# Kernel tuning notes

Measured on AMD Instinct MI355X. Metric: run time of the kernel, lower is better.

## Reference

```python
import jax, jax.numpy as jnp
import numpy as np

N = 50000   # nodes in both graphs
E = 800000  # edges per graph
IN = 128
OUT = 64
NEG_SLOPE = 0.2  # DGL GATConv default


def setup_inputs() -> dict:
    key = jax.random.key(0)
    ks = jax.random.split(key, 12)
    stdv = 1.0 / np.sqrt(OUT)
    return {
        'h': jax.random.normal(ks[0], (N, IN), dtype=jnp.float32),
        'src0': jax.random.randint(ks[1], (E,), 0, N, dtype=jnp.int32),
        'dst0': jax.random.randint(ks[2], (E,), 0, N, dtype=jnp.int32),
        'row2': jax.random.randint(ks[3], (E,), 0, N, dtype=jnp.int32),
        'col2': jax.random.randint(ks[4], (E,), 0, N, dtype=jnp.int32),
        'adj_val': jax.random.uniform(ks[5], (E,), dtype=jnp.float32),
        # GATConv params (1 head)
        'W_gat': jax.random.normal(ks[6], (IN, OUT), dtype=jnp.float32) * 0.1,
        'attn_l': jax.random.normal(ks[7], (OUT,), dtype=jnp.float32) * 0.1,
        'attn_r': jax.random.normal(ks[8], (OUT,), dtype=jnp.float32) * 0.1,
        'bias_gat': jnp.zeros((OUT,), dtype=jnp.float32),
        # GraphConvolution params
        'W_gc': jax.random.uniform(ks[9], (IN, OUT), minval=-stdv, maxval=stdv, dtype=jnp.float32),
        'bias_gc': jax.random.uniform(ks[10], (OUT,), minval=-stdv, maxval=stdv, dtype=jnp.float32),
    }


def reference(h, src0, dst0, row2, col2, adj_val, W_gat, attn_l, attn_r, bias_gat, W_gc, bias_gc):
    n = h.shape[0]
    # ---- branch 0: GATConv(1 head) + elu activation ----
    feat = h @ W_gat                        # [N, OUT]
    el = feat @ attn_l                      # [N]
    er = feat @ attn_r                      # [N]
    e = el[src0] + er[dst0]                 # [E]
    e = jnp.where(e > 0, e, NEG_SLOPE * e)  # leaky_relu
    # edge softmax over incoming edges of each dst (stable)
    m = jax.ops.segment_max(e, dst0, num_segments=n)
    ex = jnp.exp(e - m[dst0])
    s = jax.ops.segment_sum(ex, dst0, num_segments=n)
    alpha = ex / s[dst0]                    # [E]
    agg = jax.ops.segment_sum(alpha[:, None] * feat[src0], dst0, num_segments=n)
    z1 = jax.nn.elu(agg + bias_gat)         # [N, OUT]
    # ---- branch 1: GraphConvolution: elu(adj @ (h @ W) + b) ----
    support = h @ W_gc                      # [N, OUT]
    gc = jax.ops.segment_sum(adj_val[:, None] * support[col2], row2, num_segments=n)
    z2 = jax.nn.elu(gc + bias_gc)           # [N, OUT]
    # ---- semantic attention tail (forward is just split+concat) ----
    return jnp.concatenate((z1, z2), axis=1)  # [N, 2*OUT]
```

## Files before the change

kernel.cpp:

```cpp
#include <hip/hip_runtime.h>
#include <hip/hip_bf16.h>
#include <math.h>

#define IN_F 128
#define OUT_F 64
#define BKT_SH 8
#define BKT_MASK 255
#define CHUNK 4096
#define MAXTB 800
#define IDX_BITS 24
#define IDX_MASK ((1u << IDX_BITS) - 1u)
#define PAD 16

typedef __attribute__((ext_vector_type(8))) short bf16x8;
typedef __attribute__((ext_vector_type(4))) float f32x4;

__device__ inline short f2bf(float x) {
    __hip_bfloat16 b = __float2bfloat16(x);
    return *reinterpret_cast<short*>(&b);
}
__device__ inline float bflo(unsigned u) { return __uint_as_float(u << 16); }
__device__ inline float bfhi(unsigned u) { return __uint_as_float(u & 0xffff0000u); }

__global__ __launch_bounds__(256) void k_fused(const float* __restrict__ h,
                                               const float* __restrict__ Wg,
                                               const float* __restrict__ Wc,
                                               const float* __restrict__ attn_l,
                                               const float* __restrict__ attn_r,
                                               __hip_bfloat16* __restrict__ feat,
                                               __hip_bfloat16* __restrict__ support,
                                               float* __restrict__ el,
                                               float* __restrict__ er, int n, int G1,
                                               const int* __restrict__ dst0,
                                               const int* __restrict__ row2,
                                               int* __restrict__ bcnt,
                                               int* __restrict__ chunkhist,
                                               int NB, int E_) {
    __shared__ short Wl[16][128][8];
    __shared__ int hist[MAXTB];

    if ((int)blockIdx.x >= G1) {
        int TB = 2 * NB;
        int t = threadIdx.x;
        int chunk = (int)blockIdx.x - G1;
        for (int i = t; i < TB; i += 256) hist[i] = 0;
        __syncthreads();
        int e0 = chunk * CHUNK;
        for (int i = t; i < CHUNK; i += 256) {
            int e = e0 + i;
            if (e < E_) {
                atomicAdd(&hist[dst0[e] >> BKT_SH], 1);
                atomicAdd(&hist[NB + (row2[e] >> BKT_SH)], 1);
            }
        }
        __syncthreads();
        int* hrow = chunkhist + (size_t)chunk * TB;
        for (int b = t; b < TB; b += 256) {
            int c = hist[b];
            hrow[b] = c;
            if (c) atomicAdd(&bcnt[b * PAD], c);
        }
        return;
    }

    for (int i = threadIdx.x; i < 128 * 32; i += 256) {
        int k = i >> 5;
        int c4 = (i & 31) << 2;
        float4 v4 = (c4 < 64) ? *(const float4*)(Wg + k * 64 + c4)
                              : *(const float4*)(Wc + k * 64 + (c4 - 64));
        short* dst = &Wl[k >> 3][c4][k & 7];
        dst[0]  = f2bf(v4.x);
        dst[8]  = f2bf(v4.y);
        dst[16] = f2bf(v4.z);
        dst[24] = f2bf(v4.w);
    }
    __syncthreads();

    int lane = threadIdx.x & 63;
    int wv = threadIdx.x >> 6;
    int li = lane & 15, lg = lane >> 4;
    int row0 = blockIdx.x * 64 + wv * 16;

    f32x4 acc[8];
#pragma unroll
    for (int ct = 0; ct < 8; ++ct) acc[ct] = (f32x4){0.f, 0.f, 0.f, 0.f};

    int ar = row0 + li;
    if (ar >= n) ar = n - 1;
    const float* hrow = h + (size_t)ar * IN_F + lg * 8;
#pragma unroll
    for (int q = 0; q < 4; ++q) {
        float4 a0 = *(const float4*)(hrow + q * 32);
        float4 a1 = *(const float4*)(hrow + q * 32 + 4);
        bf16x8 af;
        af[0] = f2bf(a0.x); af[1] = f2bf(a0.y); af[2] = f2bf(a0.z); af[3] = f2bf(a0.w);
        af[4] = f2bf(a1.x); af[5] = f2bf(a1.y); af[6] = f2bf(a1.z); af[7] = f2bf(a1.w);
        int kg = q * 4 + lg;
#pragma unroll
        for (int ct = 0; ct < 8; ++ct) {
            bf16x8 bfr = *(const bf16x8*)&Wl[kg][ct * 16 + li][0];
            acc[ct] = __builtin_amdgcn_mfma_f32_16x16x32_bf16(af, bfr, acc[ct], 0, 0, 0);
        }
    }

    float alv[4], arv[4];
#pragma unroll
    for (int ct = 0; ct < 4; ++ct) {
        alv[ct] = attn_l[ct * 16 + li];
        arv[ct] = attn_r[ct * 16 + li];
    }
#pragma unroll
    for (int r = 0; r < 4; ++r) {
        int row = row0 + lg * 4 + r;
        float pl = 0.f, pr = 0.f;
#pragma unroll
        for (int ct = 0; ct < 4; ++ct) {
            pl += acc[ct][r] * alv[ct];
            pr += acc[ct][r] * arv[ct];
        }
#pragma unroll
        for (int m = 8; m; m >>= 1) {
            pl += __shfl_xor(pl, m);
            pr += __shfl_xor(pr, m);
        }
        if (li == 0 && row < n) { el[row] = pl; er[row] = pr; }
    }

#pragma unroll
    for (int r = 0; r < 4; ++r) {
        int row = row0 + lg * 4 + r;
        if (row >= n) continue;
#pragma unroll
        for (int ct = 0; ct < 4; ++ct)
            feat[(size_t)row * OUT_F + ct * 16 + li] = __float2bfloat16(acc[ct][r]);
#pragma unroll
        for (int ct = 4; ct < 8; ++ct)
            support[(size_t)row * OUT_F + (ct - 4) * 16 + li] = __float2bfloat16(acc[ct][r]);
    }
}

__global__ __launch_bounds__(1024) void k_part(const int* __restrict__ src0,
                                               const int* __restrict__ dst0,
                                               const int* __restrict__ row2,
                                               const int* __restrict__ col2,
                                               const float* __restrict__ adj_val,
                                               const float* __restrict__ el,
                                               const float* __restrict__ er,
                                               const int* __restrict__ bcnt,
                                               const int* __restrict__ chunkhist,
                                               int* __restrict__ gfill,
                                               int* __restrict__ boffs,
                                               int* __restrict__ offs, int tot,
                                               int2* __restrict__ tmp,
                                               int NB, int E_, int grand) {
    __shared__ int bo[MAXTB + 1];
    __shared__ int hist[MAXTB];
    __shared__ int rbase[MAXTB];
    __shared__ int sh[1024];
    int TB = 2 * NB;
    int t = threadIdx.x;

    {
        int v = (t < TB) ? bcnt[t * PAD] : 0;
        sh[t] = v;
        __syncthreads();
        for (int off = 1; off < 1024; off <<= 1) {
            int x = (t >= off) ? sh[t - off] : 0;
            __syncthreads();
            sh[t] += x;
            __syncthreads();
        }
        if (t < TB) bo[t] = sh[t] - v;
        if (t == 0) bo[TB] = grand;
    }
    __syncthreads();

    if (blockIdx.x == 0) {
        for (int b = t; b <= TB; b += 1024) boffs[b] = bo[b];
        if (t == 0) offs[tot] = grand;
    }

    const int* hrow = chunkhist + (size_t)blockIdx.x * TB;
    for (int b = t; b < TB; b += 1024) {
        int c = hrow[b];
        int bb = 0;
        if (c) bb = bo[b] + atomicAdd(&gfill[b * PAD], c);
        rbase[b] = bb;
        hist[b] = 0;
    }
    __syncthreads();
    int e0 = blockIdx.x * CHUNK;
    for (int i = t; i < CHUNK; i += 1024) {
        int e = e0 + i;
        if (e < E_) {
            int s = src0[e];
            int d = dst0[e];
            int b = d >> BKT_SH;
            int p = atomicAdd(&hist[b], 1);
            float w = el[s] + er[d];
            w = w > 0.f ? w : 0.2f * w;
            w = __expf(w);
            tmp[(size_t)rbase[b] + p] =
                make_int2((int)(((unsigned)(d & BKT_MASK) << IDX_BITS) | (unsigned)s),
                          __float_as_int(w));
            int r = row2[e];
            int b2 = NB + (r >> BKT_SH);
            int p2 = atomicAdd(&hist[b2], 1);
            tmp[(size_t)rbase[b2] + p2] =
                make_int2((int)(((unsigned)(r & BKT_MASK) << IDX_BITS) | (unsigned)col2[e]),
                          __float_as_int(adj_val[e]));
        }
    }
}

__global__ __launch_bounds__(256) void k_bbuild(const int2* __restrict__ tmp,
                                                const int* __restrict__ boffs,
                                                int* __restrict__ offs,
                                                unsigned* __restrict__ ew, int NB, int n) {
    __shared__ int hcnt[256], hoff[256], hfill[256], sh[256];
    int b = blockIdx.x;
    int t = threadIdx.x;
    int base = boffs[b];
    int cnt = boffs[b + 1] - base;
    bool isGat = b < NB;
    int nodeBase = (isGat ? b : b - NB) << BKT_SH;
    int offsBase = (isGat ? 0 : n) + nodeBase;

    hcnt[t] = 0;
    hfill[t] = 0;
    __syncthreads();
    for (int i = t; i < cnt; i += 256)
        atomicAdd(&hcnt[((unsigned)tmp[(size_t)base + i].x) >> IDX_BITS], 1);
    __syncthreads();
    sh[t] = hcnt[t];
    __syncthreads();
    for (int off = 1; off < 256; off <<= 1) {
        int x = (t >= off) ? sh[t - off] : 0;
        __syncthreads();
        sh[t] += x;
        __syncthreads();
    }
    hoff[t] = sh[t] - hcnt[t];
    if (nodeBase + t < n) offs[offsBase + t] = base + hoff[t];
    __syncthreads();
    for (int i = t; i < cnt; i += 256) {
        int2 v = tmp[(size_t)base + i];
        unsigned loc = ((unsigned)v.x) >> IDX_BITS;
        int p = atomicAdd(&hfill[loc], 1);
        unsigned idx16 = ((unsigned)v.x & IDX_MASK) & 0xffffu;
        unsigned wbits = (unsigned)(unsigned short)f2bf(__int_as_float(v.y));
        ew[(size_t)base + hoff[loc] + p] = (wbits << 16) | idx16;
    }
}

__global__ __launch_bounds__(256) void k_agg(const unsigned* __restrict__ ew,
                                             const int* __restrict__ offs,
                                             const __hip_bfloat16* __restrict__ feat,
                                             const __hip_bfloat16* __restrict__ support,
                                             const float* __restrict__ bias_gat,
                                             const float* __restrict__ bias_gc,
                                             float* __restrict__ out, int n) {
    int wave = (int)(((long long)blockIdx.x * blockDim.x + threadIdx.x) >> 6);
    int lane = threadIdx.x & 63;
    int nq = (n + 3) >> 2;
    if (wave >= 2 * nq) return;
    int q = lane >> 4;
    int fg = lane & 15;
    int qb = q << 4;

    bool isGat = wave < nq;
    int node = (isGat ? wave : wave - nq) * 4 + q;
    bool nodeValid = node < n;
    int wid = (isGat ? 0 : n) + (nodeValid ? node : 0);
    int start = offs[wid];
    int deg = nodeValid ? offs[wid + 1] - start : 0;

    const uint2* fbase = (const uint2*)(isGat ? feat : support);
    float acc[4] = {0.f, 0.f, 0.f, 0.f};
    float sw = 0.f;

    for (int c0 = 0; c0 < deg; c0 += 16) {
        int cnt = min(16, deg - c0);
        bool valid = fg < cnt;
        unsigned e = valid ? ew[(size_t)start + c0 + fg] : 0u;
        float w = bfhi(e);
        float ts = w;
        ts += __shfl_xor(ts, 1);  ts += __shfl_xor(ts, 2);
        ts += __shfl_xor(ts, 4);  ts += __shfl_xor(ts, 8);
        sw += ts;
#pragma unroll 4
        for (int k = 0; k < cnt; ++k) {
            unsigned ek = (unsigned)__shfl((int)e, qb + k);
            float wk = bfhi(ek);
            int ik = (int)(ek & 0xffffu);
            uint2 pv = fbase[(size_t)ik * 16 + fg];
            acc[0] += wk * bflo(pv.x); acc[1] += wk * bfhi(pv.x);
            acc[2] += wk * bflo(pv.y); acc[3] += wk * bfhi(pv.y);
        }
    }
    if (nodeValid) {
        float inv = isGat ? (deg > 0 ? __builtin_amdgcn_rcpf(sw) : 0.f) : 1.f;
        const float* bias = isGat ? bias_gat : bias_gc;
        int outoff = isGat ? 0 : OUT_F;
        float4 bb = *(const float4*)(bias + fg * 4);
        float z0 = acc[0] * inv + bb.x;
        float z1 = acc[1] * inv + bb.y;
        float z2 = acc[2] * inv + bb.z;
        float z3 = acc[3] * inv + bb.w;
        z0 = z0 > 0.f ? z0 : __expf(z0) - 1.f;
        z1 = z1 > 0.f ? z1 : __expf(z1) - 1.f;
        z2 = z2 > 0.f ? z2 : __expf(z2) - 1.f;
        z3 = z3 > 0.f ? z3 : __expf(z3) - 1.f;
        *(float4*)(out + (size_t)node * 128 + outoff + fg * 4) = make_float4(z0, z1, z2, z3);
    }
}

extern "C" void kernel_launch(void* const* d_in, const int* in_sizes, int n_in,
                              void* d_out, int out_size, void* d_ws, size_t ws_size,
                              hipStream_t stream) {
    const float* h        = (const float*)d_in[0];
    const int*   src0     = (const int*)d_in[1];
    const int*   dst0     = (const int*)d_in[2];
    const int*   row2     = (const int*)d_in[3];
    const int*   col2     = (const int*)d_in[4];
    const float* adj_val  = (const float*)d_in[5];
    const float* Wg       = (const float*)d_in[6];
    const float* attn_l   = (const float*)d_in[7];
    const float* attn_r   = (const float*)d_in[8];
    const float* bias_gat = (const float*)d_in[9];
    const float* Wc       = (const float*)d_in[10];
    const float* bias_gc  = (const float*)d_in[11];

    int n  = in_sizes[0] / IN_F;
    int E_ = in_sizes[1];
    float* out = (float*)d_out;

    int NB = (n + BKT_MASK) >> BKT_SH;
    int TB = 2 * NB;
    if (TB > MAXTB) return;
    if (n > 65536) return;
    if (E_ >= (1 << IDX_BITS)) return;

    int nchunk = (E_ + CHUNK - 1) / CHUNK;

    char* p = (char*)d_ws;
    auto alloc = [&](size_t bytes, size_t align) -> void* {
        size_t a = ((size_t)p + align - 1) & ~(align - 1);
        p = (char*)(a + bytes);
        return (void*)a;
    };
    size_t Rbytes = 2 * (size_t)E_ * sizeof(int2);
    if ((size_t)nchunk * TB * sizeof(int) > Rbytes) return;
    char* R = (char*)alloc(Rbytes, 256);
    int*      chunkhist = (int*)R;
    unsigned* ew        = (unsigned*)R;
    int2*  tmp   = (int2*) alloc(2 * (size_t)E_ * sizeof(int2), 256);
    int*   offs  = (int*)  alloc((2 * (size_t)n + 1) * sizeof(int), 16);
    float* el    = (float*)alloc((size_t)n * sizeof(float), 16);
    float* er    = (float*)alloc((size_t)n * sizeof(float), 16);
    int*   bcnt  = (int*)  alloc(2 * (size_t)TB * PAD * sizeof(int), 64);
    int*   gfill = bcnt + TB * PAD;
    int*   boffs = (int*)  alloc(((size_t)TB + 1) * sizeof(int), 16);
    __hip_bfloat16* feat    = (__hip_bfloat16*)alloc((size_t)n * OUT_F * sizeof(__hip_bfloat16), 256);
    __hip_bfloat16* support = (__hip_bfloat16*)alloc((size_t)n * OUT_F * sizeof(__hip_bfloat16), 256);
    size_t need = (size_t)(p - (char*)d_ws);
    if (ws_size < need) return;

    int G1 = (n + 63) / 64;

    hipMemsetAsync(bcnt, 0, 2 * (size_t)TB * PAD * sizeof(int), stream);
    k_fused<<<G1 + nchunk, 256, 0, stream>>>(h, Wg, Wc, attn_l, attn_r,
                                             feat, support, el, er, n, G1,
                                             dst0, row2, bcnt, chunkhist, NB, E_);
    k_part<<<nchunk, 1024, 0, stream>>>(src0, dst0, row2, col2, adj_val,
                                        el, er, bcnt, chunkhist, gfill,
                                        boffs, offs, 2 * n, tmp, NB, E_, 2 * E_);
    k_bbuild<<<TB, 256, 0, stream>>>(tmp, boffs, offs, ew, NB, n);
    int nq = (n + 3) >> 2;
    long long aggthreads = 2LL * nq * 64;
    k_agg<<<(int)((aggthreads + 255) / 256), 256, 0, stream>>>(
        ew, offs, feat, support, bias_gat, bias_gc, out, n);
}
```

Before: 117.0 us.

## Replace global atomic bucket offsets with per-chunk prefix scan; stage bucket build in LDS

Removes the global bcnt/gfill atomics and the memset. Each partition block now recomputes bucket totals and its own per-chunk prefix by reading the whole chunkhist table, which trades atomic contention for redundant reads of about 196x400 ints per block. The GEMM/histogram kernel moves to 512-thread blocks covering 128 rows each. Bucket build now scatters into an LDS buffer and then writes to global memory contiguously, falling back to direct scatter when a bucket is oversized.

```diff
diff --git a/kernel.cpp b/kernel.cpp
--- a/kernel.cpp
+++ b/kernel.cpp
@@ -10,7 +10,7 @@
 #define MAXTB 800
 #define IDX_BITS 24
 #define IDX_MASK ((1u << IDX_BITS) - 1u)
-#define PAD 16
+#define CAPB 6144
 
 typedef __attribute__((ext_vector_type(8))) short bf16x8;
 typedef __attribute__((ext_vector_type(4))) float f32x4;
@@ -22,7 +22,7 @@
 __device__ inline float bflo(unsigned u) { return __uint_as_float(u << 16); }
 __device__ inline float bfhi(unsigned u) { return __uint_as_float(u & 0xffff0000u); }
 
-__global__ __launch_bounds__(256) void k_fused(const float* __restrict__ h,
+__global__ __launch_bounds__(512) void k_fused(const float* __restrict__ h,
                                                const float* __restrict__ Wg,
                                                const float* __restrict__ Wc,
                                                const float* __restrict__ attn_l,
@@ -33,7 +33,6 @@
                                                float* __restrict__ er, int n, int G1,
                                                const int* __restrict__ dst0,
                                                const int* __restrict__ row2,
-                                               int* __restrict__ bcnt,
                                                int* __restrict__ chunkhist,
                                                int NB, int E_) {
     __shared__ short Wl[16][128][8];
@@ -43,10 +42,10 @@
         int TB = 2 * NB;
         int t = threadIdx.x;
         int chunk = (int)blockIdx.x - G1;
-        for (int i = t; i < TB; i += 256) hist[i] = 0;
+        for (int i = t; i < TB; i += 512) hist[i] = 0;
         __syncthreads();
         int e0 = chunk * CHUNK;
-        for (int i = t; i < CHUNK; i += 256) {
+        for (int i = t; i < CHUNK; i += 512) {
             int e = e0 + i;
             if (e < E_) {
                 atomicAdd(&hist[dst0[e] >> BKT_SH], 1);
@@ -55,15 +54,11 @@
         }
         __syncthreads();
         int* hrow = chunkhist + (size_t)chunk * TB;
-        for (int b = t; b < TB; b += 256) {
-            int c = hist[b];
-            hrow[b] = c;
-            if (c) atomicAdd(&bcnt[b * PAD], c);
-        }
+        for (int b = t; b < TB; b += 512) hrow[b] = hist[b];
         return;
     }
 
-    for (int i = threadIdx.x; i < 128 * 32; i += 256) {
+    for (int i = threadIdx.x; i < 128 * 32; i += 512) {
         int k = i >> 5;
         int c4 = (i & 31) << 2;
         float4 v4 = (c4 < 64) ? *(const float4*)(Wg + k * 64 + c4)
@@ -79,7 +74,7 @@
     int lane = threadIdx.x & 63;
     int wv = threadIdx.x >> 6;
     int li = lane & 15, lg = lane >> 4;
-    int row0 = blockIdx.x * 64 + wv * 16;
+    int row0 = blockIdx.x * 128 + wv * 16;
 
     f32x4 acc[8];
 #pragma unroll
@@ -146,50 +141,50 @@
                                                const float* __restrict__ adj_val,
                                                const float* __restrict__ el,
                                                const float* __restrict__ er,
-                                               const int* __restrict__ bcnt,
                                                const int* __restrict__ chunkhist,
-                                               int* __restrict__ gfill,
                                                int* __restrict__ boffs,
-                                               int* __restrict__ offs, int tot,
+                                               int* __restrict__ offs, int tot_nodes,
                                                int2* __restrict__ tmp,
-                                               int NB, int E_, int grand) {
+                                               int NB, int E_, int nchunk, int grand) {
     __shared__ int bo[MAXTB + 1];
     __shared__ int hist[MAXTB];
     __shared__ int rbase[MAXTB];
     __shared__ int sh[1024];
     int TB = 2 * NB;
     int t = threadIdx.x;
-
-    {
-        int v = (t < TB) ? bcnt[t * PAD] : 0;
-        sh[t] = v;
-        __syncthreads();
-        for (int off = 1; off < 1024; off <<= 1) {
-            int x = (t >= off) ? sh[t - off] : 0;
-            __syncthreads();
-            sh[t] += x;
-            __syncthreads();
-        }
-        if (t < TB) bo[t] = sh[t] - v;
-        if (t == 0) bo[TB] = grand;
-    }
-    __syncthreads();
-
-    if (blockIdx.x == 0) {
+    int myc = (int)blockIdx.x;
+
+    int pre = 0, tot = 0;
+    if (t < TB) {
+        for (int c = 0; c < nchunk; ++c) {
+            int v = chunkhist[(size_t)c * TB + t];
+            if (c < myc) pre += v;
+            tot += v;
+        }
+    }
+    sh[t] = (t < TB) ? tot : 0;
+    __syncthreads();
+    for (int off = 1; off < 1024; off <<= 1) {
+        int x = (t >= off) ? sh[t - off] : 0;
+        __syncthreads();
+        sh[t] += x;
+        __syncthreads();
+    }
+    if (t < TB) {
+        int excl = sh[t] - tot;
+        bo[t] = excl;
+        rbase[t] = excl + pre;
+        hist[t] = 0;
+    }
+    if (t == 0) bo[TB] = grand;
+    __syncthreads();
+
+    if (myc == 0) {
         for (int b = t; b <= TB; b += 1024) boffs[b] = bo[b];
-        if (t == 0) offs[tot] = grand;
-    }
-
-    const int* hrow = chunkhist + (size_t)blockIdx.x * TB;
-    for (int b = t; b < TB; b += 1024) {
-        int c = hrow[b];
-        int bb = 0;
-        if (c) bb = bo[b] + atomicAdd(&gfill[b * PAD], c);
-        rbase[b] = bb;
-        hist[b] = 0;
-    }
-    __syncthreads();
-    int e0 = blockIdx.x * CHUNK;
+        if (t == 0) offs[tot_nodes] = grand;
+    }
+
+    int e0 = myc * CHUNK;
     for (int i = t; i < CHUNK; i += 1024) {
         int e = e0 + i;
         if (e < E_) {
@@ -217,6 +212,7 @@
                                                 const int* __restrict__ boffs,
                                                 int* __restrict__ offs,
                                                 unsigned* __restrict__ ew, int NB, int n) {
+    __shared__ unsigned ew_lds[CAPB];
     __shared__ int hcnt[256], hoff[256], hfill[256], sh[256];
     int b = blockIdx.x;
     int t = threadIdx.x;
@@ -243,13 +239,27 @@
     hoff[t] = sh[t] - hcnt[t];
     if (nodeBase + t < n) offs[offsBase + t] = base + hoff[t];
     __syncthreads();
-    for (int i = t; i < cnt; i += 256) {
-        int2 v = tmp[(size_t)base + i];
-        unsigned loc = ((unsigned)v.x) >> IDX_BITS;
-        int p = atomicAdd(&hfill[loc], 1);
-        unsigned idx16 = ((unsigned)v.x & IDX_MASK) & 0xffffu;
-        unsigned wbits = (unsigned)(unsigned short)f2bf(__int_as_float(v.y));
-        ew[(size_t)base + hoff[loc] + p] = (wbits << 16) | idx16;
+    if (cnt <= CAPB) {
+        for (int i = t; i < cnt; i += 256) {
+            int2 v = tmp[(size_t)base + i];
+            unsigned loc = ((unsigned)v.x) >> IDX_BITS;
+            int p = atomicAdd(&hfill[loc], 1);
+            unsigned idx16 = ((unsigned)v.x & IDX_MASK) & 0xffffu;
+            unsigned wbits = (unsigned)(unsigned short)f2bf(__int_as_float(v.y));
+            ew_lds[hoff[loc] + p] = (wbits << 16) | idx16;
+        }
+        __syncthreads();
+        for (int i = t; i < cnt; i += 256)
+            ew[(size_t)base + i] = ew_lds[i];
+    } else {
+        for (int i = t; i < cnt; i += 256) {
+            int2 v = tmp[(size_t)base + i];
+            unsigned loc = ((unsigned)v.x) >> IDX_BITS;
+            int p = atomicAdd(&hfill[loc], 1);
+            unsigned idx16 = ((unsigned)v.x & IDX_MASK) & 0xffffu;
+            unsigned wbits = (unsigned)(unsigned short)f2bf(__int_as_float(v.y));
+            ew[(size_t)base + hoff[loc] + p] = (wbits << 16) | idx16;
+        }
     }
 }
 
@@ -358,23 +368,20 @@
     int*   offs  = (int*)  alloc((2 * (size_t)n + 1) * sizeof(int), 16);
     float* el    = (float*)alloc((size_t)n * sizeof(float), 16);
     float* er    = (float*)alloc((size_t)n * sizeof(float), 16);
-    int*   bcnt  = (int*)  alloc(2 * (size_t)TB * PAD * sizeof(int), 64);
-    int*   gfill = bcnt + TB * PAD;
     int*   boffs = (int*)  alloc(((size_t)TB + 1) * sizeof(int), 16);
     __hip_bfloat16* feat    = (__hip_bfloat16*)alloc((size_t)n * OUT_F * sizeof(__hip_bfloat16), 256);
     __hip_bfloat16* support = (__hip_bfloat16*)alloc((size_t)n * OUT_F * sizeof(__hip_bfloat16), 256);
     size_t need = (size_t)(p - (char*)d_ws);
     if (ws_size < need) return;
 
-    int G1 = (n + 63) / 64;
-
-    hipMemsetAsync(bcnt, 0, 2 * (size_t)TB * PAD * sizeof(int), stream);
-    k_fused<<<G1 + nchunk, 256, 0, stream>>>(h, Wg, Wc, attn_l, attn_r,
+    int G1 = (n + 127) / 128;
+
+    k_fused<<<G1 + nchunk, 512, 0, stream>>>(h, Wg, Wc, attn_l, attn_r,
                                              feat, support, el, er, n, G1,
-                                             dst0, row2, bcnt, chunkhist, NB, E_);
+                                             dst0, row2, chunkhist, NB, E_);
     k_part<<<nchunk, 1024, 0, stream>>>(src0, dst0, row2, col2, adj_val,
-                                        el, er, bcnt, chunkhist, gfill,
-                                        boffs, offs, 2 * n, tmp, NB, E_, 2 * E_);
+                                        el, er, chunkhist, boffs, offs, 2 * n,
+                                        tmp, NB, E_, nchunk, 2 * E_);
     k_bbuild<<<TB, 256, 0, stream>>>(tmp, boffs, offs, ew, NB, n);
     int nq = (n + 3) >> 2;
     long long aggthreads = 2LL * nq * 64;
```

New measurement: 122.8 us. +5.0%, slower.
